# Performance work log

Hardware: AMD Instinct MI355X
Metric: run time of the kernel (lower is better)

Reference implementation:

```python
import jax, jax.numpy as jnp
import numpy as np

N_NODES = 50000
N_EDGES = 600000
H = 128
LN_EPS = 1e-5


def _mlp_ln(h, w1, b1, w2, b2, w3, b3, w4, b4, g, be):
    # 4-layer MLP (Linear-ReLU x3, Linear) followed by LayerNorm, as in build_mlp
    h = jax.nn.relu(h @ w1 + b1)
    h = jax.nn.relu(h @ w2 + b2)
    h = jax.nn.relu(h @ w3 + b3)
    h = h @ w4 + b4
    mu = jnp.mean(h, axis=-1, keepdims=True)
    var = jnp.var(h, axis=-1, keepdims=True)
    return (h - mu) * jax.lax.rsqrt(var + LN_EPS) * g + be


def setup_inputs() -> dict:
    key = jax.random.key(0)
    ks = jax.random.split(key, 16)
    s = 0.02
    inp = {
        'x': jax.random.normal(ks[0], (N_NODES, H), jnp.float32),
        'edge_attr': jax.random.normal(ks[1], (N_EDGES, H), jnp.float32),
        'edge_index': jax.random.randint(ks[2], (2, N_EDGES), 0, N_NODES, jnp.int64),
        'e_w1': jax.random.normal(ks[3], (3 * H, H), jnp.float32) * s,
        'e_b1': jnp.zeros((H,), jnp.float32),
        'e_w2': jax.random.normal(ks[4], (H, H), jnp.float32) * s,
        'e_b2': jnp.zeros((H,), jnp.float32),
        'e_w3': jax.random.normal(ks[5], (H, H), jnp.float32) * s,
        'e_b3': jnp.zeros((H,), jnp.float32),
        'e_w4': jax.random.normal(ks[6], (H, H), jnp.float32) * s,
        'e_b4': jnp.zeros((H,), jnp.float32),
        'e_g': jnp.ones((H,), jnp.float32),
        'e_be': jnp.zeros((H,), jnp.float32),
        'n_w1': jax.random.normal(ks[7], (2 * H, H), jnp.float32) * s,
        'n_b1': jnp.zeros((H,), jnp.float32),
        'n_w2': jax.random.normal(ks[8], (H, H), jnp.float32) * s,
        'n_b2': jnp.zeros((H,), jnp.float32),
        'n_w3': jax.random.normal(ks[9], (H, H), jnp.float32) * s,
        'n_b3': jnp.zeros((H,), jnp.float32),
        'n_w4': jax.random.normal(ks[10], (H, H), jnp.float32) * s,
        'n_b4': jnp.zeros((H,), jnp.float32),
        'n_g': jnp.ones((H,), jnp.float32),
        'n_be': jnp.zeros((H,), jnp.float32),
    }
    return inp


def reference(x, edge_attr, edge_index,
              e_w1, e_b1, e_w2, e_b2, e_w3, e_b3, e_w4, e_b4, e_g, e_be,
              n_w1, n_b1, n_w2, n_b2, n_w3, n_b3, n_w4, n_b4, n_g, n_be):
    senders = edge_index[0]
    receivers = edge_index[1]
    # EdgeBlock: gather sender/receiver node features, concat with edge_attr -> MLP+LN
    e_in = jnp.concatenate([x[senders], x[receivers], edge_attr], axis=-1)  # [E, 3H]
    new_edge = _mlp_ln(e_in, e_w1, e_b1, e_w2, e_b2, e_w3, e_b3, e_w4, e_b4, e_g, e_be)
    # NodeBlock: scatter-add updated edge features to receiver nodes, concat with x -> MLP+LN
    agg = jax.ops.segment_sum(new_edge, receivers, num_segments=x.shape[0])  # [N, H]
    n_in = jnp.concatenate([x, agg], axis=-1)  # [N, 2H]
    new_x = _mlp_ln(n_in, n_w1, n_b1, n_w2, n_b2, n_w3, n_b3, n_w4, n_b4, n_g, n_be)
    # Residual adds (GnBlock)
    return (x + new_x, edge_attr + new_edge)
```

## Files before the change

kernel.cpp:

```cpp
#include <hip/hip_runtime.h>

#define N_NODES 50000
#define N_EDGES 600000
#define H 128

typedef __bf16 bf16x8 __attribute__((ext_vector_type(8)));
typedef float f32x4 __attribute__((ext_vector_type(4)));
typedef unsigned short u16;
typedef u16 u16x8 __attribute__((ext_vector_type(8)));
typedef u16 u16x4 __attribute__((ext_vector_type(4)));

#define MW 16384
#define WT_BYTES (11 * MW * 2)
#define XA_OFF WT_BYTES
#define NODE_B (N_NODES * H * 2)
#define XB_OFF (XA_OFF + NODE_B)
#define XN_OFF (XB_OFF + NODE_B)
#define AGG_OFF (XN_OFF + NODE_B)

__device__ inline u16 f2bf(float f) { return __builtin_bit_cast(u16, (__bf16)f); }
__device__ inline float bf2f(u16 u) {
  unsigned v = (unsigned)u << 16;
  return __builtin_bit_cast(float, v);
}

__device__ inline u16x8 cvt8(const float* __restrict__ p) {
  const float4 f0 = ((const float4*)p)[0];
  const float4 f1 = ((const float4*)p)[1];
  u16x8 o;
  o[0] = f2bf(f0.x); o[1] = f2bf(f0.y); o[2] = f2bf(f0.z); o[3] = f2bf(f0.w);
  o[4] = f2bf(f1.x); o[5] = f2bf(f1.y); o[6] = f2bf(f1.z); o[7] = f2bf(f1.w);
  return o;
}

__device__ inline f32x4 mfma_(u16x8 a, u16x8 b, f32x4 c) {
  return __builtin_amdgcn_mfma_f32_16x16x32_bf16(
      __builtin_bit_cast(bf16x8, a), __builtin_bit_cast(bf16x8, b), c, 0, 0, 0);
}


__global__ __launch_bounds__(256) void prep_weights(
    const float* __restrict__ ew1, const float* __restrict__ ew2,
    const float* __restrict__ ew3, const float* __restrict__ ew4,
    const float* __restrict__ nw1, const float* __restrict__ nw2,
    const float* __restrict__ nw3, const float* __restrict__ nw4,
    u16* __restrict__ wt)
{
  const int gid = blockIdx.x * 256 + threadIdx.x;
  if (gid >= 11 * MW) return;
  const int mat = gid >> 14, idx = gid & (MW - 1);
  const int n = idx >> 7, k = idx & 127;
  const float* src; int ro = 0; bool perm = false;
  switch (mat) {
    case 0: src = ew1; ro = 0;   break;
    case 1: src = ew1; ro = 128; break;
    case 2: src = ew1; ro = 256; break;
    case 3: src = ew2; perm = true; break;
    case 4: src = ew3; perm = true; break;
    case 5: src = ew4; perm = true; break;
    case 6: src = nw1; ro = 0;   break;
    case 7: src = nw1; ro = 128; break;
    case 8: src = nw2; perm = true; break;
    case 9: src = nw3; perm = true; break;
    default: src = nw4; perm = true; break;
  }
  int kk = k;
  if (perm) {
    const int k0 = k >> 5, kgg = (k >> 3) & 3, j = k & 7;
    kk = (k0 * 2 + (j >> 2)) * 16 + kgg * 4 + (j & 3);
  }
  wt[gid] = f2bf(src[(ro + kk) * H + n]);
}

template<int NT>
__device__ inline void layerT(const u16* __restrict__ wm,
                              const u16x8 (&bfr)[NT][4],
                              const int la, const int kg,
                              f32x4 (&acc)[NT][8])
{
#pragma unroll
  for (int t = 0; t < NT; ++t)
#pragma unroll
    for (int m = 0; m < 8; ++m) acc[t][m] = {0.f, 0.f, 0.f, 0.f};
#pragma unroll
  for (int k0 = 0; k0 < 4; ++k0) {
#pragma unroll
    for (int m = 0; m < 8; ++m) {
      const u16x8 wf = *(const u16x8*)(wm + (m * 16 + la) * 128 + k0 * 32 + kg * 8);
#pragma unroll
      for (int t = 0; t < NT; ++t)
        acc[t][m] = mfma_(wf, bfr[t][k0], acc[t][m]);
    }
  }
}

template<int NT>
__device__ inline void packT(const f32x4 (&acc)[NT][8],
                             const float* __restrict__ bias,
                             const int kg, u16x8 (&bfr)[NT][4])
{
#pragma unroll
  for (int k0 = 0; k0 < 4; ++k0) {
    const f32x4 bA = *(const f32x4*)(bias + (k0 * 2) * 16 + kg * 4);
    const f32x4 bB = *(const f32x4*)(bias + (k0 * 2 + 1) * 16 + kg * 4);
#pragma unroll
    for (int t = 0; t < NT; ++t) {
      u16x8 o;
#pragma unroll
      for (int j = 0; j < 8; ++j) {
        const int m = k0 * 2 + (j >> 2), r = j & 3;
        float v = acc[t][m][r] + ((j >> 2) ? bB[r] : bA[r]);
        v = v > 0.f ? v : 0.f;
        o[j] = f2bf(v);
      }
      bfr[t][k0] = o;
    }
  }
}

__global__ __launch_bounds__(256) void precompute(
    const float* __restrict__ x, const u16* __restrict__ wt,
    u16* __restrict__ xa, u16* __restrict__ xb, u16* __restrict__ xn)
{
  const int tid = threadIdx.x;
  const int lane = tid & 63, w = tid >> 6;
  const int n0 = blockIdx.x * 64 + w * 16;
  const int la = lane & 15, kg = lane >> 4;
  const int row = n0 + la < N_NODES ? n0 + la : N_NODES - 1;

  u16x8 bfx[1][4];
#pragma unroll
  for (int k0 = 0; k0 < 4; ++k0)
    bfx[0][k0] = cvt8(x + (size_t)row * H + k0 * 32 + kg * 8);

  const int mats[3] = {0, 1, 6};
  u16* outs[3] = {xa, xb, xn};
#pragma unroll
  for (int m3 = 0; m3 < 3; ++m3) {
    f32x4 acc[1][8];
    layerT<1>(wt + mats[m3] * MW, bfx, la, kg, acc);
    if (n0 + la < N_NODES) {
      u16* out = outs[m3] + (size_t)(n0 + la) * H;
#pragma unroll
      for (int m = 0; m < 8; ++m) {
        u16x4 o;
#pragma unroll
        for (int r = 0; r < 4; ++r) o[r] = f2bf(acc[0][m][r]);
        *(u16x4*)(out + (m >> 1) * 32 + kg * 8 + (m & 1) * 4) = o;
      }
    }
  }
}

__global__ __launch_bounds__(256, 4) void edge_kernel(
    const float* __restrict__ ea, const int* __restrict__ eidx,
    const u16* __restrict__ wt,
    const u16* __restrict__ xag, const u16* __restrict__ xbg,
    const float* __restrict__ b1, const float* __restrict__ b2,
    const float* __restrict__ b3, const float* __restrict__ b4,
    const float* __restrict__ g, const float* __restrict__ be,
    float* __restrict__ out2, float* __restrict__ agg)
{
  __shared__ float sT[4][1024];
  const int tid = threadIdx.x;
  const int lane = tid & 63, w = tid >> 6;
  const int e0 = blockIdx.x * 128 + w * 32;
  const int la = lane & 15, kg = lane >> 4;
  const int* __restrict__ snd = eidx;
  const int* __restrict__ rcv = eidx + N_EDGES;
  char* tileB = (char*)sT[w];

  int rA[2];
  rA[0] = e0 + la;      if (rA[0] >= N_EDGES) rA[0] = N_EDGES - 1;
  rA[1] = e0 + 16 + la; if (rA[1] >= N_EDGES) rA[1] = N_EDGES - 1;
  size_t sbH[2], rbH[2];
#pragma unroll
  for (int t = 0; t < 2; ++t) {
    sbH[t] = (size_t)snd[rA[t]] * H;
    rbH[t] = (size_t)rcv[rA[t]] * H;
  }

  u16x8 bfr[2][4];
#pragma unroll
  for (int t = 0; t < 2; ++t)
#pragma unroll
    for (int k0 = 0; k0 < 4; ++k0)
      bfr[t][k0] = cvt8(ea + (size_t)rA[t] * H + k0 * 32 + kg * 8);

  f32x4 acc[2][8];
  layerT<2>(wt + 2 * MW, bfr, la, kg, acc);

  u16x8 xa[2][4], xb[2][4];
#pragma unroll
  for (int t = 0; t < 2; ++t)
#pragma unroll
    for (int k0 = 0; k0 < 4; ++k0) {
      xa[t][k0] = *(const u16x8*)(xag + sbH[t] + k0 * 32 + kg * 8);
      xb[t][k0] = *(const u16x8*)(xbg + rbH[t] + k0 * 32 + kg * 8);
    }

#pragma unroll
  for (int k0 = 0; k0 < 4; ++k0) {
    const f32x4 bA = *(const f32x4*)(b1 + (k0 * 2) * 16 + kg * 4);
    const f32x4 bB = *(const f32x4*)(b1 + (k0 * 2 + 1) * 16 + kg * 4);
#pragma unroll
    for (int t = 0; t < 2; ++t) {
      u16x8 o;
#pragma unroll
      for (int j = 0; j < 8; ++j) {
        const int m = k0 * 2 + (j >> 2), r = j & 3;
        float v = acc[t][m][r] + ((j >> 2) ? bB[r] : bA[r]) +
                  bf2f(xa[t][k0][j]) + bf2f(xb[t][k0][j]);
        v = v > 0.f ? v : 0.f;
        o[j] = f2bf(v);
      }
      bfr[t][k0] = o;
    }
  }

  layerT<2>(wt + 3 * MW, bfr, la, kg, acc);
  packT<2>(acc, b2, kg, bfr);
  layerT<2>(wt + 4 * MW, bfr, la, kg, acc);
  packT<2>(acc, b3, kg, bfr);
  layerT<2>(wt + 5 * MW, bfr, la, kg, acc);

  float vs[2] = {0.f, 0.f}, vq[2] = {0.f, 0.f};
#pragma unroll
  for (int m = 0; m < 8; ++m) {
    const f32x4 b4m = *(const f32x4*)(b4 + m * 16 + kg * 4);
#pragma unroll
    for (int t = 0; t < 2; ++t)
#pragma unroll
      for (int r = 0; r < 4; ++r) {
        const float v = acc[t][m][r] + b4m[r];
        acc[t][m][r] = v;
        vs[t] += v; vq[t] += v * v;
      }
  }
#pragma unroll
  for (int t = 0; t < 2; ++t) {
    vs[t] += __shfl_xor(vs[t], 16, 64);
    vq[t] += __shfl_xor(vq[t], 16, 64);
    vs[t] += __shfl_xor(vs[t], 32, 64);
    vq[t] += __shfl_xor(vq[t], 32, 64);
  }

#pragma unroll
  for (int t = 0; t < 2; ++t) {
    const float mean = vs[t] * (1.0f / 128.0f);
    const float var = vq[t] * (1.0f / 128.0f) - mean * mean;
    const float rstd = rsqrtf(var + 1e-5f);
#pragma unroll
    for (int h = 0; h < 2; ++h) {
#pragma unroll
      for (int mm = 0; mm < 4; ++mm) {
        const int m = h * 4 + mm;
        const int co = m * 16 + kg * 4;
        const f32x4 gm = *(const f32x4*)(g + co);
        const f32x4 bem = *(const f32x4*)(be + co);
        f32x4 nv;
#pragma unroll
        for (int r = 0; r < 4; ++r)
          nv[r] = (acc[t][m][r] - mean) * rstd * gm[r] + bem[r];
        *(f32x4*)(tileB + la * 256 + ((mm * 64 + kg * 16) ^ ((la & 7) << 4))) = nv;
      }
      asm volatile("" ::: "memory");

#pragma unroll
      for (int rr = 0; rr < 4; ++rr) {
        const int trow = kg * 4 + rr;
        const int rowg = e0 + t * 16 + trow;
        if (rowg < N_EDGES) {
          const int rv = rcv[rowg];
          const size_t rb = (size_t)rowg * H;
          float* aggr = agg + (size_t)rv * H;
#pragma unroll
          for (int n = 0; n < 4; ++n) {
            const int col = h * 64 + n * 16 + la;
            const int bc = n * 64 + la * 4;
            const float ne = *(const float*)(tileB + trow * 256 + (bc ^ ((trow & 7) << 4)));
            out2[rb + col] = ea[rb + col] + ne;
            atomicAdd(aggr + col, ne);
          }
        }
      }
      asm volatile("" ::: "memory");
    }
  }
}

__global__ __launch_bounds__(256, 4) void node_kernel(
    const float* __restrict__ x, const float* __restrict__ agg,
    const u16* __restrict__ wt, const u16* __restrict__ xng,
    const float* __restrict__ b1, const float* __restrict__ b2,
    const float* __restrict__ b3, const float* __restrict__ b4,
    const float* __restrict__ g, const float* __restrict__ be,
    float* __restrict__ out1)
{
  const int tid = threadIdx.x;
  const int lane = tid & 63, w = tid >> 6;
  const int n0 = blockIdx.x * 64 + w * 16;
  const int la = lane & 15, kg = lane >> 4;
  const int row = n0 + la < N_NODES ? n0 + la : N_NODES - 1;

  u16x8 bfr[1][4];
#pragma unroll
  for (int k0 = 0; k0 < 4; ++k0)
    bfr[0][k0] = cvt8(agg + (size_t)row * H + k0 * 32 + kg * 8);
  u16x8 xn[4];
#pragma unroll
  for (int k0 = 0; k0 < 4; ++k0)
    xn[k0] = *(const u16x8*)(xng + (size_t)row * H + k0 * 32 + kg * 8);

  f32x4 acc[1][8];
  layerT<1>(wt + 7 * MW, bfr, la, kg, acc);

#pragma unroll
  for (int k0 = 0; k0 < 4; ++k0) {
    const f32x4 bA = *(const f32x4*)(b1 + (k0 * 2) * 16 + kg * 4);
    const f32x4 bB = *(const f32x4*)(b1 + (k0 * 2 + 1) * 16 + kg * 4);
    u16x8 o;
#pragma unroll
    for (int j = 0; j < 8; ++j) {
      const int m = k0 * 2 + (j >> 2), r = j & 3;
      float v = acc[0][m][r] + ((j >> 2) ? bB[r] : bA[r]) + bf2f(xn[k0][j]);
      v = v > 0.f ? v : 0.f;
      o[j] = f2bf(v);
    }
    bfr[0][k0] = o;
  }

  layerT<1>(wt + 8 * MW, bfr, la, kg, acc);
  packT<1>(acc, b2, kg, bfr);
  layerT<1>(wt + 9 * MW, bfr, la, kg, acc);
  packT<1>(acc, b3, kg, bfr);
  layerT<1>(wt + 10 * MW, bfr, la, kg, acc);

  float vs = 0.f, vq = 0.f;
#pragma unroll
  for (int m = 0; m < 8; ++m) {
    const f32x4 b4m = *(const f32x4*)(b4 + m * 16 + kg * 4);
#pragma unroll
    for (int r = 0; r < 4; ++r) {
      const float v = acc[0][m][r] + b4m[r];
      acc[0][m][r] = v;
      vs += v; vq += v * v;
    }
  }
  vs += __shfl_xor(vs, 16, 64);
  vq += __shfl_xor(vq, 16, 64);
  vs += __shfl_xor(vs, 32, 64);
  vq += __shfl_xor(vq, 32, 64);

  if (n0 + la < N_NODES) {
    const float mean = vs * (1.0f / 128.0f);
    const float var = vq * (1.0f / 128.0f) - mean * mean;
    const float rstd = rsqrtf(var + 1e-5f);
    const size_t rb = (size_t)(n0 + la) * H;
#pragma unroll
    for (int m = 0; m < 8; ++m) {
      const int co = m * 16 + kg * 4;
      const f32x4 gm = *(const f32x4*)(g + co);
      const f32x4 bem = *(const f32x4*)(be + co);
      const f32x4 xv = *(const f32x4*)(x + rb + co);
      f32x4 ov;
#pragma unroll
      for (int r = 0; r < 4; ++r)
        ov[r] = xv[r] + (acc[0][m][r] - mean) * rstd * gm[r] + bem[r];
      *(f32x4*)(out1 + rb + co) = ov;
    }
  }
}

extern "C" void kernel_launch(void* const* d_in, const int* in_sizes, int n_in,
                              void* d_out, int out_size, void* d_ws, size_t ws_size,
                              hipStream_t stream) {
  const float* x   = (const float*)d_in[0];
  const float* ea  = (const float*)d_in[1];
  const int*   ei  = (const int*)d_in[2];
  const float* ew1 = (const float*)d_in[3];
  const float* eb1 = (const float*)d_in[4];
  const float* ew2 = (const float*)d_in[5];
  const float* eb2 = (const float*)d_in[6];
  const float* ew3 = (const float*)d_in[7];
  const float* eb3 = (const float*)d_in[8];
  const float* ew4 = (const float*)d_in[9];
  const float* eb4 = (const float*)d_in[10];
  const float* eg  = (const float*)d_in[11];
  const float* ebe = (const float*)d_in[12];
  const float* nw1 = (const float*)d_in[13];
  const float* nb1 = (const float*)d_in[14];
  const float* nw2 = (const float*)d_in[15];
  const float* nb2 = (const float*)d_in[16];
  const float* nw3 = (const float*)d_in[17];
  const float* nb3 = (const float*)d_in[18];
  const float* nw4 = (const float*)d_in[19];
  const float* nb4 = (const float*)d_in[20];
  const float* ng  = (const float*)d_in[21];
  const float* nbe = (const float*)d_in[22];

  char* ws = (char*)d_ws;
  u16* wt = (u16*)ws;
  u16* xa = (u16*)(ws + XA_OFF);
  u16* xb = (u16*)(ws + XB_OFF);
  u16* xn = (u16*)(ws + XN_OFF);
  float* agg = (float*)(ws + AGG_OFF);
  float* out1 = (float*)d_out;
  float* out2 = out1 + (size_t)N_NODES * H;

  hipMemsetAsync(agg, 0, (size_t)N_NODES * H * sizeof(float), stream);
  prep_weights<<<(11 * MW + 255) / 256, 256, 0, stream>>>(
      ew1, ew2, ew3, ew4, nw1, nw2, nw3, nw4, wt);
  precompute<<<(N_NODES + 63) / 64, 256, 0, stream>>>(x, wt, xa, xb, xn);
  edge_kernel<<<(N_EDGES + 127) / 128, 256, 0, stream>>>(
      ea, ei, wt, xa, xb, eb1, eb2, eb3, eb4, eg, ebe, out2, agg);
  node_kernel<<<(N_NODES + 63) / 64, 256, 0, stream>>>(
      x, agg, wt, xn, nb1, nb2, nb3, nb4, ng, nbe, out1);
}
```

Before: 840.1 us.

## Privatize scatter-add accumulation into multiple partial buffers selected by block

```diff
diff --git a/kernel.cpp b/kernel.cpp
--- a/kernel.cpp
+++ b/kernel.cpp
@@ -3,6 +3,7 @@
 #define N_NODES 50000
 #define N_EDGES 600000
 #define H 128
+#define NODE_ELEMS (N_NODES * H)
 
 typedef __bf16 bf16x8 __attribute__((ext_vector_type(8)));
 typedef float f32x4 __attribute__((ext_vector_type(4)));
@@ -27,6 +28,24 @@
 __device__ inline u16x8 cvt8(const float* __restrict__ p) {
   const float4 f0 = ((const float4*)p)[0];
   const float4 f1 = ((const float4*)p)[1];
+  u16x8 o;
+  o[0] = f2bf(f0.x); o[1] = f2bf(f0.y); o[2] = f2bf(f0.z); o[3] = f2bf(f0.w);
+  o[4] = f2bf(f1.x); o[5] = f2bf(f1.y); o[6] = f2bf(f1.z); o[7] = f2bf(f1.w);
+  return o;
+}
+
+template<int NPART>
+__device__ inline u16x8 cvt8sum(const float* __restrict__ p) {
+  float4 f0 = ((const float4*)p)[0];
+  float4 f1 = ((const float4*)p)[1];
+#pragma unroll
+  for (int q = 1; q < NPART; ++q) {
+    const float* pp = p + (size_t)q * NODE_ELEMS;
+    const float4 a0 = ((const float4*)pp)[0];
+    const float4 a1 = ((const float4*)pp)[1];
+    f0.x += a0.x; f0.y += a0.y; f0.z += a0.z; f0.w += a0.w;
+    f1.x += a1.x; f1.y += a1.y; f1.z += a1.z; f1.w += a1.w;
+  }
   u16x8 o;
   o[0] = f2bf(f0.x); o[1] = f2bf(f0.y); o[2] = f2bf(f0.z); o[3] = f2bf(f0.w);
   o[4] = f2bf(f1.x); o[5] = f2bf(f1.y); o[6] = f2bf(f1.z); o[7] = f2bf(f1.w);
@@ -152,6 +171,7 @@
   }
 }
 
+template<int NPART>
 __global__ __launch_bounds__(256, 4) void edge_kernel(
     const float* __restrict__ ea, const int* __restrict__ eidx,
     const u16* __restrict__ wt,
@@ -169,6 +189,8 @@
   const int* __restrict__ snd = eidx;
   const int* __restrict__ rcv = eidx + N_EDGES;
   char* tileB = (char*)sT[w];
+  float* __restrict__ aggP =
+      agg + (size_t)(blockIdx.x & (NPART - 1)) * NODE_ELEMS;
 
   int rA[2];
   rA[0] = e0 + la;      if (rA[0] >= N_EDGES) rA[0] = N_EDGES - 1;
@@ -273,7 +295,7 @@
         if (rowg < N_EDGES) {
           const int rv = rcv[rowg];
           const size_t rb = (size_t)rowg * H;
-          float* aggr = agg + (size_t)rv * H;
+          float* aggr = aggP + (size_t)rv * H;
 #pragma unroll
           for (int n = 0; n < 4; ++n) {
             const int col = h * 64 + n * 16 + la;
@@ -289,6 +311,7 @@
   }
 }
 
+template<int NPART>
 __global__ __launch_bounds__(256, 4) void node_kernel(
     const float* __restrict__ x, const float* __restrict__ agg,
     const u16* __restrict__ wt, const u16* __restrict__ xng,
@@ -306,7 +329,7 @@
   u16x8 bfr[1][4];
 #pragma unroll
   for (int k0 = 0; k0 < 4; ++k0)
-    bfr[0][k0] = cvt8(agg + (size_t)row * H + k0 * 32 + kg * 8);
+    bfr[0][k0] = cvt8sum<NPART>(agg + (size_t)row * H + k0 * 32 + kg * 8);
   u16x8 xn[4];
 #pragma unroll
   for (int k0 = 0; k0 < 4; ++k0)
@@ -408,12 +431,29 @@
   float* out1 = (float*)d_out;
   float* out2 = out1 + (size_t)N_NODES * H;
 
-  hipMemsetAsync(agg, 0, (size_t)N_NODES * H * sizeof(float), stream);
   prep_weights<<<(11 * MW + 255) / 256, 256, 0, stream>>>(
       ew1, ew2, ew3, ew4, nw1, nw2, nw3, nw4, wt);
   precompute<<<(N_NODES + 63) / 64, 256, 0, stream>>>(x, wt, xa, xb, xn);
-  edge_kernel<<<(N_EDGES + 127) / 128, 256, 0, stream>>>(
-      ea, ei, wt, xa, xb, eb1, eb2, eb3, eb4, eg, ebe, out2, agg);
-  node_kernel<<<(N_NODES + 63) / 64, 256, 0, stream>>>(
-      x, agg, wt, xn, nb1, nb2, nb3, nb4, ng, nbe, out1);
-}
+
+  const size_t need8 = (size_t)AGG_OFF + 8ull * NODE_ELEMS * 4;
+  const size_t need4 = (size_t)AGG_OFF + 4ull * NODE_ELEMS * 4;
+  if (ws_size >= need8) {
+    hipMemsetAsync(agg, 0, 8ull * NODE_ELEMS * 4, stream);
+    edge_kernel<8><<<(N_EDGES + 127) / 128, 256, 0, stream>>>(
+        ea, ei, wt, xa, xb, eb1, eb2, eb3, eb4, eg, ebe, out2, agg);
+    node_kernel<8><<<(N_NODES + 63) / 64, 256, 0, stream>>>(
+        x, agg, wt, xn, nb1, nb2, nb3, nb4, ng, nbe, out1);
+  } else if (ws_size >= need4) {
+    hipMemsetAsync(agg, 0, 4ull * NODE_ELEMS * 4, stream);
+    edge_kernel<4><<<(N_EDGES + 127) / 128, 256, 0, stream>>>(
+        ea, ei, wt, xa, xb, eb1, eb2, eb3, eb4, eg, ebe, out2, agg);
+    node_kernel<4><<<(N_NODES + 63) / 64, 256, 0, stream>>>(
+        x, agg, wt, xn, nb1, nb2, nb3, nb4, ng, nbe, out1);
+  } else {
+    hipMemsetAsync(agg, 0, (size_t)NODE_ELEMS * 4, stream);
+    edge_kernel<1><<<(N_EDGES + 127) / 128, 256, 0, stream>>>(
+        ea, ei, wt, xa, xb, eb1, eb2, eb3, eb4, eg, ebe, out2, agg);
+    node_kernel<1><<<(N_NODES + 63) / 64, 256, 0, stream>>>(
+        x, agg, wt, xn, nb1, nb2, nb3, nb4, ng, nbe, out1);
+  }
+}
```

Measured after the change: 1.005 ms. +19.6%, slower.
